# Performance work log

Hardware: AMD Instinct MI355X
Metric: run time of the kernel (lower is better)

The kernel has to match this reference:

```python
import jax, jax.numpy as jnp
import numpy as np

N_CLUSTERS = 64
COLLAPSE_REG = 0.1
H_SMOOTH = -0.0001
H_ALPHA = 0.0001
H_LAMBDA = 0.0001


def setup_inputs() -> dict:
    key = jax.random.key(0)
    ks = jax.random.split(key, 6)
    n, d, k = 65536, 512, N_CLUSTERS
    e0 = 1048576  # directed edges before symmetrization
    features = jax.random.normal(ks[0], (n, d), jnp.float32)
    s = jax.random.randint(ks[1], (e0,), 0, n)
    t = jax.random.randint(ks[2], (e0,), 0, n)
    v = jax.random.uniform(ks[3], (e0,), jnp.float32)
    # symmetrize adjacency (real graph datasets are undirected -> L = D - A is PSD)
    edge_src = jnp.concatenate([s, t]).astype(jnp.int64)
    edge_dst = jnp.concatenate([t, s]).astype(jnp.int64)
    edge_vals = jnp.concatenate([v, v])
    W = jax.random.normal(ks[4], (d, k), jnp.float32) / np.sqrt(d).astype(np.float32)
    b = jnp.zeros((k,), jnp.float32)
    return dict(features=features, edge_src=edge_src, edge_dst=edge_dst,
                edge_vals=edge_vals, W=W, b=b)


def reference(features, edge_src, edge_dst, edge_vals, W, b):
    n, d = features.shape
    k = W.shape[1]
    # assignments = softmax(Dense(features))
    S = jax.nn.softmax(features @ W + b, axis=1)  # [n,k]
    cluster_sizes = jnp.sum(S, axis=0)            # [k]
    S_pool = S / cluster_sizes                    # [n,k]
    # sparse column-degree (tf.sparse.reduce_sum axis=0) and edge count
    deg_col = jax.ops.segment_sum(edge_vals, edge_dst, num_segments=n)[:, None]  # [n,1]
    m = jnp.sum(deg_col)
    # A @ S via edge-list gather/scatter (sparse_dense_matmul)
    AS = jax.ops.segment_sum(edge_vals[:, None] * S[edge_dst], edge_src,
                             num_segments=n)      # [n,k]
    graph_pooled = AS.T @ S                       # S^T A S, [k,k]
    normalizer = ((S.T @ deg_col) @ (deg_col.T @ S)) / 2.0 / m  # [k,k]
    spectral_loss = -jnp.trace(graph_pooled - normalizer) / 2.0 / m
    collapse_loss = (jnp.linalg.norm(cluster_sizes) / n
                     * jnp.sqrt(jnp.float32(k)) - 1.0)
    # pooled features
    FP = jax.nn.selu(S_pool.T @ features)         # [k,d]
    # FGC loss chain: Laplacian L = D_row - A applied sparsely
    deg_row = jax.ops.segment_sum(edge_vals, edge_src, num_segments=n)[:, None]
    LS = deg_row * S - AS                         # L @ S, [n,k]
    StLS = LS.T @ S                               # smoothness1 = S^T L S, [k,k]
    # log(det(StLS + ones)) computed stably via slogdet (det is positive: PSD + rank-1)
    _sign, logabsdet = jnp.linalg.slogdet(StLS + jnp.ones_like(StLS))
    smoothness_loss = logabsdet * H_SMOOTH
    # trace((L S) @ FP @ FP^T): trace of [n,k] matrix = sum of first k diagonal entries
    trace_loss = jnp.einsum('ic,cd,id->', LS[:k], FP, FP)
    frob_loss = jnp.linalg.norm(S @ FP - features) * H_ALPHA
    one_two_loss = jnp.linalg.norm(jnp.sum(jnp.abs(S), axis=0)) * H_LAMBDA
    fgc_loss = smoothness_loss + trace_loss + frob_loss + one_two_loss
    total_loss = spectral_loss + COLLAPSE_REG * collapse_loss + fgc_loss
    return FP, S, total_loss
```

## Files before the change

kernel.cpp:

```cpp
#include <hip/hip_runtime.h>
#include <hip/hip_bf16.h>
#include <cstdint>
#include <cstddef>

typedef unsigned short u16;
typedef float f32x4 __attribute__((ext_vector_type(4)));
typedef short bf16x8 __attribute__((ext_vector_type(8)));
typedef unsigned short u16x8 __attribute__((ext_vector_type(8)));

__device__ __forceinline__ u16 f2bf(float f) {
    uint32_t u = __float_as_uint(f);
    u += 0x7fffu + ((u >> 16) & 1u);
    return (u16)(u >> 16);
}
__device__ __forceinline__ float bf2f(u16 h) {
    return __uint_as_float(((uint32_t)h) << 16);
}

#define SWZ(c) ((((c) ^ ((c) >> 3)) & 7) << 2)

__global__ __launch_bounds__(256) void k_prep(const float* __restrict__ Wg, u16* __restrict__ Wt) {
    int idx = blockIdx.x * 256 + threadIdx.x;
    int k = idx >> 6, c = idx & 63;
    int lin = c * 512 + (k ^ ((c & 7) << 3));
    Wt[lin] = f2bf(Wg[idx]);
}

__global__ __launch_bounds__(256) void k1(const float* __restrict__ F,
    const u16* __restrict__ WtG, const float* __restrict__ bias,
    float* __restrict__ S_out, u16* __restrict__ Sbf,
    float* __restrict__ sizes, float* __restrict__ scal) {
    __shared__ __align__(16) u16 Wl[64 * 512];
    __shared__ __align__(16) u16 Al[64 * 64];
    __shared__ float red4[4];
    const int tid = threadIdx.x;
    const int row0 = blockIdx.x * 64;
    for (int j = tid; j < 4096; j += 256)
        ((uint4*)Wl)[j] = ((const uint4*)WtG)[j];

    const int lane = tid & 63;
    const int wv = __builtin_amdgcn_readfirstlane(tid >> 6);
    const int l15 = lane & 15, lq = lane >> 4;
    f32x4 acc[4];
    #pragma unroll
    for (int tn = 0; tn < 4; tn++)
        #pragma unroll
        for (int e = 0; e < 4; e++) acc[tn][e] = 0.f;
    float sumf2 = 0.f;
    const int sr = tid >> 2, skq = tid & 3;
    const int sw = (sr & 7) << 3;

    for (int k0 = 0; k0 < 512; k0 += 64) {
        const float* fp = F + (size_t)(row0 + sr) * 512 + k0 + skq * 16;
        float4 v[4];
        u16 h[16];
        #pragma unroll
        for (int q = 0; q < 4; q++) v[q] = ((const float4*)fp)[q];
        #pragma unroll
        for (int q = 0; q < 4; q++) {
            sumf2 += v[q].x * v[q].x + v[q].y * v[q].y + v[q].z * v[q].z + v[q].w * v[q].w;
            h[q * 4 + 0] = f2bf(v[q].x); h[q * 4 + 1] = f2bf(v[q].y);
            h[q * 4 + 2] = f2bf(v[q].z); h[q * 4 + 3] = f2bf(v[q].w);
        }
        #pragma unroll
        for (int half = 0; half < 2; half++) {
            u16x8 pk;
            #pragma unroll
            for (int e2 = 0; e2 < 8; e2++) pk[e2] = h[half * 8 + e2];
            *(u16x8*)&Al[sr * 64 + ((skq * 16 + half * 8) ^ sw)] = pk;
        }
        __syncthreads();
        #pragma unroll
        for (int kk = 0; kk < 64; kk += 32) {
            const int arow = wv * 16 + l15;
            bf16x8 a = *(const bf16x8*)&Al[arow * 64 + ((kk + lq * 8) ^ ((arow & 7) << 3))];
            #pragma unroll
            for (int tn = 0; tn < 4; tn++) {
                const int bc = tn * 16 + l15;
                bf16x8 b = *(const bf16x8*)&Wl[bc * 512 + ((k0 + kk + lq * 8) ^ ((bc & 7) << 3))];
                acc[tn] = __builtin_amdgcn_mfma_f32_16x16x32_bf16(a, b, acc[tn], 0, 0, 0);
            }
        }
        __syncthreads();
    }

    float bias4[4], szacc[4] = {0.f, 0.f, 0.f, 0.f};
    #pragma unroll
    for (int tn = 0; tn < 4; tn++) bias4[tn] = bias[tn * 16 + l15];
    #pragma unroll
    for (int r2 = 0; r2 < 4; r2++) {
        float L[4];
        #pragma unroll
        for (int tn = 0; tn < 4; tn++) L[tn] = acc[tn][r2] + bias4[tn];
        float mx = fmaxf(fmaxf(L[0], L[1]), fmaxf(L[2], L[3]));
        #pragma unroll
        for (int mm = 1; mm < 16; mm <<= 1) mx = fmaxf(mx, __shfl_xor(mx, mm));
        float e[4], s = 0.f;
        #pragma unroll
        for (int tn = 0; tn < 4; tn++) { e[tn] = __expf(L[tn] - mx); s += e[tn]; }
        #pragma unroll
        for (int mm = 1; mm < 16; mm <<= 1) s += __shfl_xor(s, mm);
        const float inv = 1.f / s;
        const size_t grow = (size_t)(row0 + wv * 16 + lq * 4 + r2);
        #pragma unroll
        for (int tn = 0; tn < 4; tn++) {
            const float svl = e[tn] * inv;
            S_out[grow * 64 + tn * 16 + l15] = svl;
            Sbf[grow * 64 + tn * 16 + l15] = f2bf(svl);
            szacc[tn] += svl;
        }
    }
    #pragma unroll
    for (int tn = 0; tn < 4; tn++) {
        float vs = szacc[tn];
        vs += __shfl_xor(vs, 16);
        vs += __shfl_xor(vs, 32);
        if (lq == 0) atomicAdd(sizes + tn * 16 + l15, vs);
    }
    #pragma unroll
    for (int mm = 1; mm < 64; mm <<= 1) sumf2 += __shfl_xor(sumf2, mm);
    if (lane == 0) red4[wv] = sumf2;
    __syncthreads();
    if (tid == 0) atomicAdd(scal + 1, red4[0] + red4[1] + red4[2] + red4[3]);
}

__global__ __launch_bounds__(512) void k_sweep(const int* __restrict__ esrc,
    const int* __restrict__ edst, const float* __restrict__ ev,
    const u16* __restrict__ Sbf, const float* __restrict__ S, const int E2,
    float* __restrict__ GP8, float* __restrict__ SDS8, float* __restrict__ u8,
    float* __restrict__ AS64, float* __restrict__ deg64, float* __restrict__ scal) {
    __shared__ uint32_t Tl[2][2048];
    __shared__ uint32_t Pl[2][2048];
    __shared__ uint32_t Ql[2][2048];
    __shared__ uint32_t Rl[2][2048];
    const int tid = threadIdx.x;
    const int lane = tid & 63;
    const int wv = __builtin_amdgcn_readfirstlane(tid >> 6);
    const int l15 = lane & 15, lq = lane >> 4;
    const int xcd = blockIdx.x & 7;
    float* __restrict__ GPmy = GP8 + (size_t)xcd * 4096;
    float* __restrict__ SDSmy = SDS8 + (size_t)xcd * 4096;
    float* __restrict__ umy = u8 + (size_t)xcd * 64;

    const bool isP = tid < 256;
    const int st = tid & 255;
    const int p = st >> 3, g = st & 7;
    float vsum = 0.f;
    float uacc[8];
    #pragma unroll
    for (int j = 0; j < 8; j++) uacc[j] = 0.f;

    f32x4 aG[2], aS[2];
    #pragma unroll
    for (int t = 0; t < 2; t++)
        #pragma unroll
        for (int r = 0; r < 4; r++) { aG[t][r] = 0.f; aS[t][r] = 0.f; }

    const int ma = 16 * (wv & 3) + l15;
    const int aoff = ma * 32, aswz = SWZ(ma);
    const int nb0 = 32 * (wv >> 2) + l15;
    const int nb1 = nb0 + 16;
    const int b0off = nb0 * 32, b0swz = SWZ(nb0);
    const int b1off = nb1 * 32, b1swz = SWZ(nb1);

    const int nch = E2 >> 6;
    const int stride = gridDim.x;
    int ch = blockIdx.x;
    if (ch >= nch) return;

    int2 ia_c, ib_c;
    float2 vv_c;
    {
        const int e0 = (ch << 6) + 2 * p;
        ia_c = isP ? *(const int2*)&edst[e0] : *(const int2*)&esrc[e0];
        ib_c = isP ? *(const int2*)&esrc[e0] : *(const int2*)&edst[e0];
        vv_c = *(const float2*)&ev[e0];
    }
    u16x8 ra_c = *(const u16x8*)&Sbf[(size_t)ia_c.x * 64 + 8 * g];
    u16x8 rb_c = *(const u16x8*)&Sbf[(size_t)ia_c.y * 64 + 8 * g];

    int buf = 0;
    while (true) {
        if (isP) {
            #pragma unroll
            for (int j = 0; j < 8; j++) {
                const int c = 8 * g + j;
                const int off = c * 32 + (p ^ SWZ(c));
                Tl[buf][off] = (uint32_t)(u16)ra_c[j] | ((uint32_t)(u16)rb_c[j] << 16);
                Pl[buf][off] = (uint32_t)f2bf(vv_c.x * bf2f((u16)ra_c[j])) |
                               ((uint32_t)f2bf(vv_c.y * bf2f((u16)rb_c[j])) << 16);
            }
        } else {
            #pragma unroll
            for (int j = 0; j < 8; j++) {
                const int c = 8 * g + j;
                const int off = c * 32 + (p ^ SWZ(c));
                Ql[buf][off] = (uint32_t)(u16)ra_c[j] | ((uint32_t)(u16)rb_c[j] << 16);
                Rl[buf][off] = (uint32_t)f2bf(vv_c.x * bf2f((u16)ra_c[j])) |
                               ((uint32_t)f2bf(vv_c.y * bf2f((u16)rb_c[j])) << 16);
            }
        }
        #pragma unroll
        for (int j = 0; j < 8; j++)
            uacc[j] = fmaf(vv_c.x, bf2f((u16)ra_c[j]),
                      fmaf(vv_c.y, bf2f((u16)rb_c[j]), uacc[j]));
        if (!isP && g == 0) vsum += vv_c.x + vv_c.y;
        if (g == 0) {
            if (ib_c.x < 64) atomicAdd(deg64 + ib_c.x, vv_c.x);
            if (ib_c.y < 64) atomicAdd(deg64 + ib_c.y, vv_c.y);
        }
        if (ib_c.x < 64) {
            const float4 fa = *(const float4*)(S + (size_t)ia_c.x * 64 + 8 * g);
            const float4 fb = *(const float4*)(S + (size_t)ia_c.x * 64 + 8 * g + 4);
            float* dst = AS64 + ib_c.x * 64 + 8 * g;
            atomicAdd(dst + 0, vv_c.x * fa.x); atomicAdd(dst + 1, vv_c.x * fa.y);
            atomicAdd(dst + 2, vv_c.x * fa.z); atomicAdd(dst + 3, vv_c.x * fa.w);
            atomicAdd(dst + 4, vv_c.x * fb.x); atomicAdd(dst + 5, vv_c.x * fb.y);
            atomicAdd(dst + 6, vv_c.x * fb.z); atomicAdd(dst + 7, vv_c.x * fb.w);
        }
        if (ib_c.y < 64) {
            const float4 fa = *(const float4*)(S + (size_t)ia_c.y * 64 + 8 * g);
            const float4 fb = *(const float4*)(S + (size_t)ia_c.y * 64 + 8 * g + 4);
            float* dst = AS64 + ib_c.y * 64 + 8 * g;
            atomicAdd(dst + 0, vv_c.y * fa.x); atomicAdd(dst + 1, vv_c.y * fa.y);
            atomicAdd(dst + 2, vv_c.y * fa.z); atomicAdd(dst + 3, vv_c.y * fa.w);
            atomicAdd(dst + 4, vv_c.y * fb.x); atomicAdd(dst + 5, vv_c.y * fb.y);
            atomicAdd(dst + 6, vv_c.y * fb.z); atomicAdd(dst + 7, vv_c.y * fb.w);
        }
        const int chn = ch + stride;
        const int chc = chn < nch ? chn : (nch - 1);
        int2 ia_n, ib_n;
        float2 vv_n;
        {
            const int e0 = (chc << 6) + 2 * p;
            ia_n = isP ? *(const int2*)&edst[e0] : *(const int2*)&esrc[e0];
            ib_n = isP ? *(const int2*)&esrc[e0] : *(const int2*)&edst[e0];
            vv_n = *(const float2*)&ev[e0];
        }
        const u16x8 ra_n = *(const u16x8*)&Sbf[(size_t)ia_n.x * 64 + 8 * g];
        const u16x8 rb_n = *(const u16x8*)&Sbf[(size_t)ia_n.y * 64 + 8 * g];
        __syncthreads();
        #pragma unroll
        for (int half = 0; half < 2; half++) {
            const int w0 = half * 16 + lq * 4;
            const bf16x8 afP = *(const bf16x8*)&Pl[buf][aoff + (w0 ^ aswz)];
            const bf16x8 afR = *(const bf16x8*)&Rl[buf][aoff + (w0 ^ aswz)];
            const bf16x8 qb0 = *(const bf16x8*)&Ql[buf][b0off + (w0 ^ b0swz)];
            const bf16x8 qb1 = *(const bf16x8*)&Ql[buf][b1off + (w0 ^ b1swz)];
            const bf16x8 tb0 = *(const bf16x8*)&Tl[buf][b0off + (w0 ^ b0swz)];
            const bf16x8 tb1 = *(const bf16x8*)&Tl[buf][b1off + (w0 ^ b1swz)];
            aG[0] = __builtin_amdgcn_mfma_f32_16x16x32_bf16(afP, qb0, aG[0], 0, 0, 0);
            aG[1] = __builtin_amdgcn_mfma_f32_16x16x32_bf16(afP, qb1, aG[1], 0, 0, 0);
            aS[0] = __builtin_amdgcn_mfma_f32_16x16x32_bf16(afR, qb0, aS[0], 0, 0, 0);
            aS[1] = __builtin_amdgcn_mfma_f32_16x16x32_bf16(afR, qb1, aS[1], 0, 0, 0);
            aS[0] = __builtin_amdgcn_mfma_f32_16x16x32_bf16(afP, tb0, aS[0], 0, 0, 0);
            aS[1] = __builtin_amdgcn_mfma_f32_16x16x32_bf16(afP, tb1, aS[1], 0, 0, 0);
        }
        ch = chn;
        if (ch >= nch) break;
        ia_c = ia_n; ib_c = ib_n; vv_c = vv_n; ra_c = ra_n; rb_c = rb_n;
        buf ^= 1;
    }
    #pragma unroll
    for (int t = 0; t < 2; t++)
        #pragma unroll
        for (int r = 0; r < 4; r++) {
            const int c1 = 16 * (wv & 3) + 4 * lq + r;
            const int c2 = 32 * (wv >> 2) + 16 * t + l15;
            atomicAdd(GPmy + c1 * 64 + c2, aG[t][r]);
            atomicAdd(SDSmy + c1 * 64 + c2, aS[t][r]);
        }
    #pragma unroll
    for (int j = 0; j < 8; j++) {
        uacc[j] += __shfl_xor(uacc[j], 8);
        uacc[j] += __shfl_xor(uacc[j], 16);
        uacc[j] += __shfl_xor(uacc[j], 32);
    }
    if (lane < 8) {
        #pragma unroll
        for (int j = 0; j < 8; j++)
            atomicAdd(umy + 8 * lane + j, uacc[j]);
    }
    if (wv >= 4) {
        #pragma unroll
        for (int mm = 1; mm < 64; mm <<= 1) vsum += __shfl_xor(vsum, mm);
        if (lane == 0) atomicAdd(scal + 0, vsum + vsum);
    }
}

__global__ __launch_bounds__(256) void k_mrg(const float* __restrict__ GP8,
    const float* __restrict__ SDS8, const float* __restrict__ u8,
    float* __restrict__ GP, float* __restrict__ SDS, float* __restrict__ u_vec) {
    const int bid = blockIdx.x;
    const int t = threadIdx.x;
    if (bid < 16) {
        const int j = bid * 256 + t;
        const int jt = (j & 63) * 64 + (j >> 6);
        float s = 0.f;
        #pragma unroll
        for (int c = 0; c < 8; c++)
            s += GP8[(size_t)c * 4096 + j] + GP8[(size_t)c * 4096 + jt];
        GP[j] = s;
    } else if (bid < 32) {
        const int j = (bid - 16) * 256 + t;
        float s = 0.f;
        #pragma unroll
        for (int c = 0; c < 8; c++) s += SDS8[(size_t)c * 4096 + j];
        SDS[j] = s;
    } else if (t < 64) {
        float s = 0.f;
        #pragma unroll
        for (int c = 0; c < 8; c++) s += u8[c * 64 + t];
        u_vec[t] = s;
    }
}

__global__ __launch_bounds__(256) void k2m(const float* __restrict__ F,
    const u16* __restrict__ Sbf, float* __restrict__ G) {
    __shared__ uint32_t Ss[64 * 32];
    __shared__ uint32_t Fs[128 * 32];
    const int tid = threadIdx.x;
    const int lane = tid & 63;
    const int wv = __builtin_amdgcn_readfirstlane(tid >> 6);
    const int l15 = lane & 15, lq = lane >> 4;
    const int d0 = (blockIdx.x & 3) * 128;
    const int kblk = blockIdx.x >> 2;

    f32x4 acc[8];
    #pragma unroll
    for (int t8 = 0; t8 < 8; t8++)
        #pragma unroll
        for (int r = 0; r < 4; r++) acc[t8][r] = 0.f;

    const int s_ip = tid >> 3;
    const int s_cs = (tid & 7) * 8;
    const int f_dg = tid & 31;
    const int f_ipb = tid >> 5;

    for (int ch = 0; ch < 8; ch++) {
        const int i0 = kblk * 512 + ch * 64;
        {
            const u16x8 r0 = *(const u16x8*)&Sbf[(size_t)(i0 + 2 * s_ip) * 64 + s_cs];
            const u16x8 r1 = *(const u16x8*)&Sbf[(size_t)(i0 + 2 * s_ip + 1) * 64 + s_cs];
            #pragma unroll
            for (int j = 0; j < 8; j++) {
                const int c = s_cs + j;
                const uint32_t pk = (uint32_t)(u16)r0[j] | ((uint32_t)(u16)r1[j] << 16);
                Ss[c * 32 + (s_ip ^ (((c >> 2) & 7) << 2))] = pk;
            }
        }
        #pragma unroll
        for (int s = 0; s < 4; s++) {
            const int ip = f_ipb + 8 * s;
            const float4 a = *(const float4*)(F + (size_t)(i0 + 2 * ip) * 512 + d0 + 4 * f_dg);
            const float4 b = *(const float4*)(F + (size_t)(i0 + 2 * ip + 1) * 512 + d0 + 4 * f_dg);
            const float al[4] = {a.x, a.y, a.z, a.w};
            const float bl[4] = {b.x, b.y, b.z, b.w};
            #pragma unroll
            for (int j = 0; j < 4; j++) {
                const int d = 4 * f_dg + j;
                const uint32_t pk = (uint32_t)f2bf(al[j]) | ((uint32_t)f2bf(bl[j]) << 16);
                Fs[d * 32 + (ip ^ (((d >> 2) & 7) << 2))] = pk;
            }
        }
        __syncthreads();
        #pragma unroll
        for (int kk = 0; kk < 64; kk += 32) {
            const int w0 = (kk >> 1) + (lq << 2);
            const int ca = 16 * wv + l15;
            const bf16x8 afrag = *(const bf16x8*)&Ss[ca * 32 + (w0 ^ (((ca >> 2) & 7) << 2))];
            #pragma unroll
            for (int t8 = 0; t8 < 8; t8++) {
                const int d = 16 * t8 + l15;
                const bf16x8 bfrag = *(const bf16x8*)&Fs[d * 32 + (w0 ^ (((d >> 2) & 7) << 2))];
                acc[t8] = __builtin_amdgcn_mfma_f32_16x16x32_bf16(afrag, bfrag, acc[t8], 0, 0, 0);
            }
        }
        __syncthreads();
    }
    #pragma unroll
    for (int t8 = 0; t8 < 8; t8++) {
        #pragma unroll
        for (int r = 0; r < 4; r++) {
            const int c = 16 * wv + 4 * lq + r;
            const int d = d0 + 16 * t8 + l15;
            atomicAdd(G + (size_t)c * 512 + d, acc[t8][r]);
        }
    }
}

__global__ __launch_bounds__(256) void k_kk(const u16* __restrict__ Sbf,
    float* __restrict__ SS) {
    __shared__ float Pss[4][16][64];
    const int tid = threadIdx.x, lane = tid & 63;
    const int wv = __builtin_amdgcn_readfirstlane(tid >> 6);
    const int cs = blockIdx.x & 3, c0 = cs * 16;
    const int rbase = (blockIdx.x >> 2) * 512 + wv * 128;
    float ss[16];
    #pragma unroll
    for (int cc = 0; cc < 16; cc++) ss[cc] = 0.f;
    for (int r = 0; r < 128; r++) {
        const int i = rbase + r;
        const float sv = bf2f(Sbf[(size_t)i * 64 + lane]);
        const u16* srow = Sbf + (size_t)i * 64 + c0;
        #pragma unroll
        for (int cc = 0; cc < 16; cc++)
            ss[cc] = fmaf(bf2f(srow[cc]), sv, ss[cc]);
    }
    #pragma unroll
    for (int cc = 0; cc < 16; cc++) Pss[wv][cc][lane] = ss[cc];
    __syncthreads();
    for (int q = 0; q < 4; q++) {
        const int cell = tid * 4 + q, cc = cell >> 6, l = cell & 63;
        atomicAdd(SS + (c0 + cc) * 64 + l,
                  Pss[0][cc][l] + Pss[1][cc][l] + Pss[2][cc][l] + Pss[3][cc][l]);
    }
}

__device__ __forceinline__ float bred256(float v, float* red) {
    #pragma unroll
    for (int mm = 1; mm < 64; mm <<= 1) v += __shfl_xor(v, mm);
    const int t = threadIdx.x;
    __syncthreads();
    if ((t & 63) == 0) red[t >> 6] = v;
    __syncthreads();
    return red[0] + red[1] + red[2] + red[3];
}

__global__ __launch_bounds__(256) void k_fp(const float* __restrict__ G,
    const float* __restrict__ sizes, float* __restrict__ FP, float* __restrict__ scal) {
    __shared__ float red[4];
    const int idx = blockIdx.x * 256 + threadIdx.x;
    const int c = idx >> 9;
    const float g = G[idx];
    const float x = g / sizes[c];
    const float fp = 1.0507009873554805f * (x > 0.f ? x : 1.6732632423543772f * (__expf(x) - 1.f));
    FP[idx] = fp;
    const float gd = bred256(g * fp, red);
    if (threadIdx.x == 0) atomicAdd(scal + 2, gd);
}

__global__ __launch_bounds__(256) void k_fft(const float* __restrict__ FP, float* __restrict__ FFt) {
    __shared__ float red[256];
    const int c = blockIdx.x;
    const int cp = threadIdx.x & 63, part = threadIdx.x >> 6;
    float a = 0.f;
    const int dbase = part * 128;
    for (int dd = 0; dd < 128; dd++)
        a = fmaf(FP[c * 512 + dbase + dd], FP[cp * 512 + dbase + dd], a);
    red[threadIdx.x] = a;
    __syncthreads();
    if (threadIdx.x < 64)
        FFt[c * 64 + threadIdx.x] = red[threadIdx.x] + red[threadIdx.x + 64] +
                                    red[threadIdx.x + 128] + red[threadIdx.x + 192];
}

__global__ __launch_bounds__(64) void k_lu(const float* __restrict__ SDS,
    const float* __restrict__ GP, float* __restrict__ scal) {
    __shared__ float M[64][65];
    const int l = threadIdx.x;
    for (int c = 0; c < 64; c++) M[l][c] = SDS[l * 64 + c] - GP[l * 64 + c] + 1.0f;
    __syncthreads();
    float logdet = 0.f;
    for (int k = 0; k < 64; k++) {
        float v = (l >= k) ? fabsf(M[l][k]) : -1.f;
        int idx = l;
        #pragma unroll
        for (int mm = 1; mm < 64; mm <<= 1) {
            const float ov = __shfl_xor(v, mm);
            const int oi = __shfl_xor(idx, mm);
            if (ov > v || (ov == v && oi < idx)) { v = ov; idx = oi; }
        }
        if (idx != k) {
            const float t1 = M[k][l], t2 = M[idx][l];
            __syncthreads();
            M[k][l] = t2;
            M[idx][l] = t1;
        }
        __syncthreads();
        const float piv = M[k][k];
        logdet += logf(fabsf(piv));
        if (l > k) {
            const float f = M[l][k] / piv;
            for (int c = k + 1; c < 64; c++) M[l][c] = fmaf(-f, M[k][c], M[l][c]);
        }
        __syncthreads();
    }
    if (l == 0) scal[3] = logdet;
}

__global__ __launch_bounds__(256) void k_final(const float* __restrict__ GP,
    const float* __restrict__ SS, const float* __restrict__ FFt, const float* __restrict__ u_vec,
    const float* __restrict__ sizes, const float* __restrict__ deg64,
    const float* __restrict__ AS64, const float* __restrict__ S,
    const float* __restrict__ scal, float* __restrict__ out_loss, const float fn) {
    __shared__ float red[4];
    const int t = threadIdx.x;
    float sA = 0.f, trl = 0.f, trg = 0.f, u2 = 0.f, sz2 = 0.f;
    for (int q = t; q < 4096; q += 256) sA += SS[q] * FFt[q];
    for (int q = t; q < 4096; q += 256) {
        const int i = q >> 6, c = q & 63;
        const float ls = deg64[i] * S[i * 64 + c] - AS64[q];
        trl += ls * FFt[c * 64 + i];
    }
    if (t < 64) { trg = GP[t * 65]; u2 = u_vec[t] * u_vec[t]; sz2 = sizes[t] * sizes[t]; }
    sA = bred256(sA, red);
    trl = bred256(trl, red);
    trg = bred256(trg, red);
    u2 = bred256(u2, red);
    sz2 = bred256(sz2, red);
    if (t == 0) {
        const float m = scal[0], sumF2 = scal[1], gfp = scal[2], lad = scal[3];
        const float spectral = -(trg - u2 / (2.f * m)) / (2.f * m);
        const float collapse = sqrtf(sz2) / fn * 8.f - 1.f;
        const float frob = sqrtf(fmaxf(sA - 2.f * gfp + sumF2, 0.f)) * 1e-4f;
        const float one_two = sqrtf(sz2) * 1e-4f;
        const float smooth = lad * (-1e-4f);
        out_loss[0] = spectral + 0.1f * collapse + smooth + trl + frob + one_two;
    }
}

extern "C" void kernel_launch(void* const* d_in, const int* in_sizes, int n_in,
                              void* d_out, int out_size, void* d_ws, size_t ws_size,
                              hipStream_t stream) {
    const float* F = (const float*)d_in[0];
    const int* esrc = (const int*)d_in[1];
    const int* edst = (const int*)d_in[2];
    const float* ev = (const float*)d_in[3];
    const float* Wg = (const float*)d_in[4];
    const float* bg = (const float*)d_in[5];
    const int n = in_sizes[0] / 512;
    const int E = in_sizes[1];
    const int E2 = E >> 1;

    float* outF = (float*)d_out;
    float* outS = outF + 64 * 512;
    float* outL = outS + (size_t)n * 64;

    char* w = (char*)d_ws;
    float* sizes = (float*)w;
    float* u_vec = sizes + 64;
    float* scal = u_vec + 64;
    float* G = scal + 64;
    float* SS = G + 64 * 512;
    float* AS64 = SS + 4096;
    float* deg64 = AS64 + 4096;
    float* GP8 = deg64 + 64;
    float* SDS8 = GP8 + 8 * 4096;
    float* u8 = SDS8 + 8 * 4096;
    char* zend = (char*)(u8 + 512);
    const size_t zero_bytes = (size_t)(zend - w);
    float* GP = (float*)zend;
    float* SDS = GP + 4096;
    float* FFt = SDS + 4096;
    u16* Sbf = (u16*)(FFt + 4096);
    u16* Wt = Sbf + (size_t)n * 64;

    hipMemsetAsync(d_ws, 0, zero_bytes, stream);
    k_prep<<<128, 256, 0, stream>>>(Wg, Wt);
    k1<<<n / 64, 256, 0, stream>>>(F, Wt, bg, outS, Sbf, sizes, scal);
    k_sweep<<<512, 512, 0, stream>>>(esrc, edst, ev, Sbf, outS, E2, GP8, SDS8, u8, AS64, deg64, scal);
    k2m<<<512, 256, 0, stream>>>(F, Sbf, G);
    k_mrg<<<33, 256, 0, stream>>>(GP8, SDS8, u8, GP, SDS, u_vec);
    k_kk<<<(n / 512) * 4, 256, 0, stream>>>(Sbf, SS);
    k_fp<<<128, 256, 0, stream>>>(G, sizes, outF, scal);
    k_fft<<<64, 256, 0, stream>>>(outF, FFt);
    k_lu<<<1, 64, 0, stream>>>(SDS, GP, scal);
    k_final<<<1, 256, 0, stream>>>(GP, SS, FFt, u_vec, sizes, deg64, AS64, outS, scal, outL, (float)n);
}
```

Measured before the change: 530.1 us.

## Single-buffer sweep LDS and double the sweep grid for occupancy

Drops the double-buffered shared-memory staging in the edge sweep kernel to a single buffer, which halves its LDS footprint (64KB to 32KB) at the cost of an extra barrier per chunk. The grid is doubled from 512 to 1024 blocks so more blocks can be resident per CU and hide gather latency. The added barrier serializes the staging writes with the MFMA reads, and a larger grid means more per-block atomic flushes into the partial accumulators.

```diff
diff --git a/kernel.cpp b/kernel.cpp
--- a/kernel.cpp
+++ b/kernel.cpp
@@ -129,10 +129,10 @@
     const u16* __restrict__ Sbf, const float* __restrict__ S, const int E2,
     float* __restrict__ GP8, float* __restrict__ SDS8, float* __restrict__ u8,
     float* __restrict__ AS64, float* __restrict__ deg64, float* __restrict__ scal) {
-    __shared__ uint32_t Tl[2][2048];
-    __shared__ uint32_t Pl[2][2048];
-    __shared__ uint32_t Ql[2][2048];
-    __shared__ uint32_t Rl[2][2048];
+    __shared__ uint32_t Tl[2048];
+    __shared__ uint32_t Pl[2048];
+    __shared__ uint32_t Ql[2048];
+    __shared__ uint32_t Rl[2048];
     const int tid = threadIdx.x;
     const int lane = tid & 63;
     const int wv = __builtin_amdgcn_readfirstlane(tid >> 6);
@@ -179,25 +179,24 @@
     u16x8 ra_c = *(const u16x8*)&Sbf[(size_t)ia_c.x * 64 + 8 * g];
     u16x8 rb_c = *(const u16x8*)&Sbf[(size_t)ia_c.y * 64 + 8 * g];
 
-    int buf = 0;
     while (true) {
         if (isP) {
             #pragma unroll
             for (int j = 0; j < 8; j++) {
                 const int c = 8 * g + j;
                 const int off = c * 32 + (p ^ SWZ(c));
-                Tl[buf][off] = (uint32_t)(u16)ra_c[j] | ((uint32_t)(u16)rb_c[j] << 16);
-                Pl[buf][off] = (uint32_t)f2bf(vv_c.x * bf2f((u16)ra_c[j])) |
-                               ((uint32_t)f2bf(vv_c.y * bf2f((u16)rb_c[j])) << 16);
+                Tl[off] = (uint32_t)(u16)ra_c[j] | ((uint32_t)(u16)rb_c[j] << 16);
+                Pl[off] = (uint32_t)f2bf(vv_c.x * bf2f((u16)ra_c[j])) |
+                          ((uint32_t)f2bf(vv_c.y * bf2f((u16)rb_c[j])) << 16);
             }
         } else {
             #pragma unroll
             for (int j = 0; j < 8; j++) {
                 const int c = 8 * g + j;
                 const int off = c * 32 + (p ^ SWZ(c));
-                Ql[buf][off] = (uint32_t)(u16)ra_c[j] | ((uint32_t)(u16)rb_c[j] << 16);
-                Rl[buf][off] = (uint32_t)f2bf(vv_c.x * bf2f((u16)ra_c[j])) |
-                               ((uint32_t)f2bf(vv_c.y * bf2f((u16)rb_c[j])) << 16);
+                Ql[off] = (uint32_t)(u16)ra_c[j] | ((uint32_t)(u16)rb_c[j] << 16);
+                Rl[off] = (uint32_t)f2bf(vv_c.x * bf2f((u16)ra_c[j])) |
+                          ((uint32_t)f2bf(vv_c.y * bf2f((u16)rb_c[j])) << 16);
             }
         }
         #pragma unroll
@@ -243,12 +242,12 @@
         #pragma unroll
         for (int half = 0; half < 2; half++) {
             const int w0 = half * 16 + lq * 4;
-            const bf16x8 afP = *(const bf16x8*)&Pl[buf][aoff + (w0 ^ aswz)];
-            const bf16x8 afR = *(const bf16x8*)&Rl[buf][aoff + (w0 ^ aswz)];
-            const bf16x8 qb0 = *(const bf16x8*)&Ql[buf][b0off + (w0 ^ b0swz)];
-            const bf16x8 qb1 = *(const bf16x8*)&Ql[buf][b1off + (w0 ^ b1swz)];
-            const bf16x8 tb0 = *(const bf16x8*)&Tl[buf][b0off + (w0 ^ b0swz)];
-            const bf16x8 tb1 = *(const bf16x8*)&Tl[buf][b1off + (w0 ^ b1swz)];
+            const bf16x8 afP = *(const bf16x8*)&Pl[aoff + (w0 ^ aswz)];
+            const bf16x8 afR = *(const bf16x8*)&Rl[aoff + (w0 ^ aswz)];
+            const bf16x8 qb0 = *(const bf16x8*)&Ql[b0off + (w0 ^ b0swz)];
+            const bf16x8 qb1 = *(const bf16x8*)&Ql[b1off + (w0 ^ b1swz)];
+            const bf16x8 tb0 = *(const bf16x8*)&Tl[b0off + (w0 ^ b0swz)];
+            const bf16x8 tb1 = *(const bf16x8*)&Tl[b1off + (w0 ^ b1swz)];
             aG[0] = __builtin_amdgcn_mfma_f32_16x16x32_bf16(afP, qb0, aG[0], 0, 0, 0);
             aG[1] = __builtin_amdgcn_mfma_f32_16x16x32_bf16(afP, qb1, aG[1], 0, 0, 0);
             aS[0] = __builtin_amdgcn_mfma_f32_16x16x32_bf16(afR, qb0, aS[0], 0, 0, 0);
@@ -259,7 +258,7 @@
         ch = chn;
         if (ch >= nch) break;
         ia_c = ia_n; ib_c = ib_n; vv_c = vv_n; ra_c = ra_n; rb_c = rb_n;
-        buf ^= 1;
+        __syncthreads();
     }
     #pragma unroll
     for (int t = 0; t < 2; t++)
@@ -559,7 +558,7 @@
     hipMemsetAsync(d_ws, 0, zero_bytes, stream);
     k_prep<<<128, 256, 0, stream>>>(Wg, Wt);
     k1<<<n / 64, 256, 0, stream>>>(F, Wt, bg, outS, Sbf, sizes, scal);
-    k_sweep<<<512, 512, 0, stream>>>(esrc, edst, ev, Sbf, outS, E2, GP8, SDS8, u8, AS64, deg64, scal);
+    k_sweep<<<1024, 512, 0, stream>>>(esrc, edst, ev, Sbf, outS, E2, GP8, SDS8, u8, AS64, deg64, scal);
     k2m<<<512, 256, 0, stream>>>(F, Sbf, G);
     k_mrg<<<33, 256, 0, stream>>>(GP8, SDS8, u8, GP, SDS, u_vec);
     k_kk<<<(n / 512) * 4, 256, 0, stream>>>(Sbf, SS);
```

Result: slower. 626.6 us (+18.2%).
